# Kernel optimization log

Measured on AMD Instinct MI355X. Metric: run time of the kernel, lower is better.

The kernel has to match this reference:

```python
import jax, jax.numpy as jnp
import numpy as np

K = 3  # kernel_size


def conv2d_same(x, w, b):
    # x: NHWC, w: HWIO
    y = jax.lax.conv_general_dilated(
        x, w, window_strides=(1, 1), padding='SAME',
        dimension_numbers=('NHWC', 'HWIO', 'NHWC'))
    return y + b


def setup_inputs() -> dict:
    key = jax.random.key(0)
    k0, k1, k2 = jax.random.split(key, 3)
    B, H, Wd, C, F = 8, 128, 128, 64, 128
    x = jax.random.normal(k0, (B, H, Wd, C), jnp.float32)
    # offset conv: small random weights (zeros in original init -> degenerate),
    # scaled down so offsets stay in a realistic few-pixel range
    W_off = jax.random.normal(k1, (K, K, C, 2 * K * K), jnp.float32) * 0.01
    b_off = jnp.zeros((2 * K * K,), jnp.float32)
    fan_in = K * K * K * K * C
    W = jax.random.normal(k2, (K, K, K * K * C, F), jnp.float32) / np.float32(np.sqrt(fan_in))
    b = jnp.zeros((F,), jnp.float32)
    return {"x": x, "W_off": W_off, "b_off": b_off, "W": W, "b": b}


def reference(x, W_off, b_off, W, b):
    B, H, Wd, C = x.shape
    KK = K * K
    # predicted per-pixel, per-tap (dx, dy) offsets
    offsets = conv2d_same(x, W_off, b_off).reshape(B, H, Wd, KK, 2)

    # base pixel grid, stacked as (x, y) like the original
    gy, gx = jnp.meshgrid(jnp.arange(H, dtype=jnp.float32),
                          jnp.arange(Wd, dtype=jnp.float32), indexing='ij')
    grid = jnp.stack([gx, gy], axis=-1)[None, :, :, None, :]  # (1,H,W,1,2)

    # kernel tap grid, 'xy' meshgrid like tf.meshgrid default
    off = (K - 1) / 2.0
    lin = jnp.linspace(-off, off, K).astype(jnp.float32)
    kx, ky = jnp.meshgrid(lin, lin)
    kgrid = jnp.stack([kx, ky], axis=-1).reshape(1, 1, 1, KK, 2)

    loc = grid + kgrid + offsets  # (B,H,W,KK,2)
    lx = jnp.clip(loc[..., 0], 0.0, Wd - 1.0)
    ly = jnp.clip(loc[..., 1], 0.0, H - 1.0)

    x0 = jnp.clip(jnp.floor(lx), 0.0, Wd - 1.0)
    x1 = jnp.clip(jnp.floor(lx) + 1.0, 0.0, Wd - 1.0)
    y0 = jnp.clip(jnp.floor(ly), 0.0, H - 1.0)
    y1 = jnp.clip(jnp.floor(ly) + 1.0, 0.0, H - 1.0)

    # weights computed from the CLIPPED corner coords, as in the original
    wa = (x1 - lx) * (y1 - ly)
    wb = (x1 - lx) * (ly - y0)
    wc = (lx - x0) * (y1 - ly)
    wd = (lx - x0) * (ly - y0)

    x0i, x1i = x0.astype(jnp.int32), x1.astype(jnp.int32)
    y0i, y1i = y0.astype(jnp.int32), y1.astype(jnp.int32)

    xf = x.reshape(B, H * Wd, C)

    def gather(yi, xi):
        idx = (yi * Wd + xi).reshape(B, -1)           # (B, H*W*KK)
        g = jax.vmap(lambda f, i: f[i])(xf, idx)      # (B, P, C)
        return g.reshape(B, H, Wd, KK, C)

    Ia = gather(y0i, x0i)
    Ib = gather(y1i, x0i)
    Ic = gather(y0i, x1i)
    Id = gather(y1i, x1i)

    sampled = (wa[..., None] * Ia + wb[..., None] * Ib
               + wc[..., None] * Ic + wd[..., None] * Id)
    sampled = sampled.reshape(B, H, Wd, KK * C)
    return conv2d_same(sampled, W, b)
```

## Files before the change

kernel.cpp:

```cpp
#include <hip/hip_runtime.h>
#include <hip/hip_bf16.h>

#define B_   8
#define H_   128
#define W_   128
#define C_   64
#define F_   128
#define KDIM 5184
#define BHW_ 131072

#define TH   8
#define TW   16
#define HY   10
#define HX   18
#define NPX  180

#define STILE 0
#define BTILE 11520
#define PARMW 36096
#define PARMO 37536
#define LDSSZ 38976

typedef __bf16 bf16x8 __attribute__((ext_vector_type(8)));
typedef float  f32x4  __attribute__((ext_vector_type(4)));

__device__ __forceinline__ unsigned short f2bf(float f) {
  unsigned int u = __float_as_uint(f);
  unsigned int r = (u + 0x7fffu + ((u >> 16) & 1u)) >> 16;
  return (unsigned short)r;
}

__global__ __launch_bounds__(256) void woff_prep_kernel(
    const float* __restrict__ Woff, unsigned short* __restrict__ WbHi,
    unsigned short* __restrict__ WbLo) {
  int u = blockIdx.x * 256 + threadIdx.x;
  if (u >= 18432) return;
  int j  = u & 7;
  int kq = (u >> 3) & 3;
  int n  = (u >> 5) & 15;
  int nt = (u >> 9) & 1;
  int tc = u >> 10;
  int tap = tc >> 1, kch = tc & 1;
  int o = nt * 16 + n;
  int c = kch * 32 + kq * 8 + j;
  float val = 0.f;
  if (o < 18) val = Woff[(tap * 64 + c) * 18 + o];
  unsigned short h = f2bf(val);
  float hf = __uint_as_float((unsigned)h << 16);
  WbHi[u] = h;
  WbLo[u] = f2bf(val - hf);
}

__global__ __launch_bounds__(256, 3) void offs_mfma_kernel(
    const float* __restrict__ x, const unsigned short* __restrict__ WbHi,
    const unsigned short* __restrict__ WbLo, const float* __restrict__ boff,
    float* __restrict__ offsP) {
  __shared__ __align__(16) short lds[26112];
  const int tid = threadIdx.x, lane = tid & 63, w = tid >> 6;
  const int bid = blockIdx.x;
  const int b  = bid >> 7;
  const int t  = bid & 127;
  const int r4 = t >> 2, cq = t & 3;
  const int gy0 = r4 * 4, gx0 = cq * 32;
  const float* xb = x + (size_t)b * (H_ * W_ * C_);

#pragma unroll
  for (int it = 0; it < 7; ++it) {
    int u = it * 256 + tid;
    if (u < 1632) {
      int p = u >> 3, j = u & 7;
      int rowi = p / 34, coli = p - rowi * 34;
      int gy = gy0 - 1 + rowi, gx = gx0 - 1 + coli;
      union { unsigned short s[8]; uint4 v; } hi, lo;
      if ((unsigned)gy < (unsigned)H_ && (unsigned)gx < (unsigned)W_) {
        const float* src = xb + (((gy << 7) + gx) << 6) + j * 8;
        float4 v0 = ((const float4*)src)[0], v1 = ((const float4*)src)[1];
        float f[8] = {v0.x, v0.y, v0.z, v0.w, v1.x, v1.y, v1.z, v1.w};
#pragma unroll
        for (int e = 0; e < 8; ++e) {
          unsigned short h16 = f2bf(f[e]);
          hi.s[e] = h16;
          lo.s[e] = f2bf(f[e] - __uint_as_float((unsigned)h16 << 16));
        }
      } else {
        hi.v = make_uint4(0, 0, 0, 0);
        lo.v = hi.v;
      }
      int a = p * 64 + ((j ^ (coli & 7)) * 8);
      *(uint4*)&lds[a] = hi.v;
      *(uint4*)&lds[13056 + a] = lo.v;
    }
  }
  __syncthreads();

  const int l15 = lane & 15, kq = lane >> 4;
  const int bbase = (l15 * 4 + kq) * 8;
  f32x4 acc[2][2] = {};

#pragma unroll
  for (int ky = 0; ky < 3; ++ky) {
#pragma unroll
    for (int kx = 0; kx < 3; ++kx) {
      const int tap = ky * 3 + kx;
#pragma unroll
      for (int kch = 0; kch < 2; ++kch) {
        const int tc = tap * 2 + kch;
        bf16x8 bh0 = *(const bf16x8*)&WbHi[tc * 1024 + bbase];
        bf16x8 bh1 = *(const bf16x8*)&WbHi[tc * 1024 + 512 + bbase];
        bf16x8 bl0 = *(const bf16x8*)&WbLo[tc * 1024 + bbase];
        bf16x8 bl1 = *(const bf16x8*)&WbLo[tc * 1024 + 512 + bbase];
#pragma unroll
        for (int mt = 0; mt < 2; ++mt) {
          int coli = mt * 16 + l15 + kx;
          int px = (w + ky) * 34 + coli;
          int a = px * 64 + (((kch * 4 + kq) ^ (coli & 7)) * 8);
          bf16x8 ah = *(const bf16x8*)&lds[a];
          bf16x8 al = *(const bf16x8*)&lds[13056 + a];
          acc[mt][0] = __builtin_amdgcn_mfma_f32_16x16x32_bf16(ah, bh0, acc[mt][0], 0, 0, 0);
          acc[mt][0] = __builtin_amdgcn_mfma_f32_16x16x32_bf16(al, bh0, acc[mt][0], 0, 0, 0);
          acc[mt][0] = __builtin_amdgcn_mfma_f32_16x16x32_bf16(ah, bl0, acc[mt][0], 0, 0, 0);
          acc[mt][1] = __builtin_amdgcn_mfma_f32_16x16x32_bf16(ah, bh1, acc[mt][1], 0, 0, 0);
          acc[mt][1] = __builtin_amdgcn_mfma_f32_16x16x32_bf16(al, bh1, acc[mt][1], 0, 0, 0);
          acc[mt][1] = __builtin_amdgcn_mfma_f32_16x16x32_bf16(ah, bl1, acc[mt][1], 0, 0, 0);
        }
      }
    }
  }

  __syncthreads();
  float* accbuf = (float*)lds;
  float bv0 = boff[l15];
  float bv1 = boff[min(16 + l15, 17)];
#pragma unroll
  for (int mt = 0; mt < 2; ++mt)
#pragma unroll
    for (int r = 0; r < 4; ++r) {
      int px = mt * 16 + kq * 4 + r;
      accbuf[(w * 32 + px) * 19 + l15] = acc[mt][0][r] + bv0;
      if (l15 < 2)
        accbuf[(w * 32 + px) * 19 + 16 + l15] = acc[mt][1][r] + bv1;
    }
  __syncthreads();
  const int lane32 = tid & 31, tpi = tid >> 5;
#pragma unroll
  for (int v = 0; v < 9; ++v) {
    int u = v * 8 + tpi;
    int o = u >> 2, w2 = u & 3;
    float val = accbuf[(w2 * 32 + lane32) * 19 + o];
    offsP[(size_t)o * BHW_ + (size_t)b * 16384 + (gy0 + w2) * 128 + gx0 + lane32] = val;
  }
}

__global__ __launch_bounds__(256) void wt_prep_kernel(
    const float* __restrict__ Wf, unsigned short* __restrict__ Wt) {
  __shared__ float Wl[64][65];
  const int tid = threadIdx.x;
  const int kk0 = (blockIdx.x % 81) * 64;
  const int f0  = (blockIdx.x / 81) * 64;
  for (int i = tid; i < 4096; i += 256) {
    int kk = i >> 6, f = i & 63;
    Wl[kk][f] = Wf[(size_t)(kk0 + kk) * F_ + f0 + f];
  }
  __syncthreads();
  for (int i = tid; i < 4096; i += 256) {
    int f = i >> 6, kk = i & 63;
    Wt[(size_t)(f0 + f) * KDIM + kk0 + kk] = f2bf(Wl[kk][f]);
  }
}

__global__ __launch_bounds__(256, 2) void fused_kernel(
    const float* __restrict__ x, const float* __restrict__ offsP,
    const unsigned short* __restrict__ Wt, const float* __restrict__ bias,
    float* __restrict__ out) {
  __shared__ __align__(16) short lds[LDSSZ];
  const int tid  = threadIdx.x;
  const int lane = tid & 63;
  const int wv   = tid >> 6;
  const int gr   = (blockIdx.x & 7) * 128 + (blockIdx.x >> 3);
  const int b    = gr >> 7;
  const int tile = gr & 127;
  const int ty   = tile >> 3, tx = tile & 7;
  const int gy0  = ty * TH, gx0 = tx * TW;
  const float* xb = x + (size_t)b * (H_ * W_ * C_);

  const int l15  = lane & 15, quad = lane >> 4;
  const int sub  = lane & 7,  rig  = lane >> 3;
  const int wn   = (wv & 1) * 64;

  f32x4 acc[4][4] = {};

  int p0[4];
#pragma unroll
  for (int i = 0; i < 4; ++i) p0[i] = ((wv >> 1) * 4 + i) * HX + l15;
  int bo[2][4];
#pragma unroll
  for (int ks = 0; ks < 2; ++ks)
#pragma unroll
    for (int j = 0; j < 4; ++j)
      bo[ks][j] = BTILE + (wn + 16 * j + l15) * 64 + (((ks * 4 + quad) ^ (l15 & 7)) * 8);

  const int s_py = tid / HX, s_px = tid - s_py * HX;

  for (int t = 0; t < 9; ++t) {
    __syncthreads();
#pragma unroll
    for (int i = 0; i < 12; ++i) {
      int slot = wv * 12 + i;
      int chunk = slot >> 4;
      int f = ((slot & 15) * 8) + rig;
      const short* src = (const short*)Wt + (size_t)f * KDIM +
                         chunk * 576 + t * 64 + ((sub ^ rig) * 8);
      __builtin_amdgcn_global_load_lds(
          (const __attribute__((address_space(1))) void*)src,
          (__attribute__((address_space(3))) void*)&lds[BTILE + slot * 512],
          16, 0, 0);
    }
    if (tid < NPX) {
      int gy = gy0 + s_py - 1, gx = gx0 + s_px - 1;
      float wa = 0.f, wb = 0.f, wc = 0.f, wd = 0.f;
      int oA = 0, oB = 0, oC = 0, oD = 0;
      if ((unsigned)gy < (unsigned)H_ && (unsigned)gx < (unsigned)W_) {
        int pix = (b * H_ + gy) * W_ + gx;
        float offx = offsP[(size_t)(2 * t) * BHW_ + pix];
        float offy = offsP[(size_t)(2 * t + 1) * BHW_ + pix];
        float lx = (float)gx + (float)(t % 3 - 1) + offx;
        float ly = (float)gy + (float)(t / 3 - 1) + offy;
        lx = fminf(fmaxf(lx, 0.f), 127.f);
        ly = fminf(fmaxf(ly, 0.f), 127.f);
        float fx = floorf(lx), fy = floorf(ly);
        float x0c = fminf(fmaxf(fx, 0.f), 127.f);
        float x1c = fminf(fmaxf(fx + 1.f, 0.f), 127.f);
        float y0c = fminf(fmaxf(fy, 0.f), 127.f);
        float y1c = fminf(fmaxf(fy + 1.f, 0.f), 127.f);
        wa = (x1c - lx) * (y1c - ly);
        wb = (x1c - lx) * (ly - y0c);
        wc = (lx - x0c) * (y1c - ly);
        wd = (lx - x0c) * (ly - y0c);
        int ix0 = (int)x0c, ix1 = (int)x1c, iy0 = (int)y0c, iy1 = (int)y1c;
        oA = (iy0 * W_ + ix0) * C_;
        oB = (iy1 * W_ + ix0) * C_;
        oC = (iy0 * W_ + ix1) * C_;
        oD = (iy1 * W_ + ix1) * C_;
      }
      ((float4*)&lds[PARMW])[tid] = make_float4(wa, wb, wc, wd);
      ((int4*)&lds[PARMO])[tid]  = make_int4(oA | (s_px << 20), oB, oC, oD);
    }
    __syncthreads();
#pragma unroll
    for (int it = 0; it < 6; ++it) {
      int u = it * 256 + tid;
      if (u < NPX * 8) {
        int p = u >> 3, j = u & 7;
        float4 wv4 = ((const float4*)&lds[PARMW])[p];
        int4   ov4 = ((const int4*)&lds[PARMO])[p];
        int pxl = ov4.x >> 20;
        const float* pa = xb + (ov4.x & 0xFFFFF) + j * 8;
        const float* pb = xb + ov4.y + j * 8;
        const float* pc = xb + ov4.z + j * 8;
        const float* pd = xb + ov4.w + j * 8;
        float4 A0 = ((const float4*)pa)[0], A1 = ((const float4*)pa)[1];
        float4 B0 = ((const float4*)pb)[0], B1 = ((const float4*)pb)[1];
        float4 C0 = ((const float4*)pc)[0], C1 = ((const float4*)pc)[1];
        float4 D0 = ((const float4*)pd)[0], D1 = ((const float4*)pd)[1];
        union { __bf16 h[8]; uint4 v; } uu;
        uu.h[0] = (__bf16)(wv4.x * A0.x + wv4.y * B0.x + wv4.z * C0.x + wv4.w * D0.x);
        uu.h[1] = (__bf16)(wv4.x * A0.y + wv4.y * B0.y + wv4.z * C0.y + wv4.w * D0.y);
        uu.h[2] = (__bf16)(wv4.x * A0.z + wv4.y * B0.z + wv4.z * C0.z + wv4.w * D0.z);
        uu.h[3] = (__bf16)(wv4.x * A0.w + wv4.y * B0.w + wv4.z * C0.w + wv4.w * D0.w);
        uu.h[4] = (__bf16)(wv4.x * A1.x + wv4.y * B1.x + wv4.z * C1.x + wv4.w * D1.x);
        uu.h[5] = (__bf16)(wv4.x * A1.y + wv4.y * B1.y + wv4.z * C1.y + wv4.w * D1.y);
        uu.h[6] = (__bf16)(wv4.x * A1.z + wv4.y * B1.z + wv4.z * C1.z + wv4.w * D1.z);
        uu.h[7] = (__bf16)(wv4.x * A1.w + wv4.y * B1.w + wv4.z * C1.w + wv4.w * D1.w);
        *(uint4*)&lds[STILE + p * 64 + ((j ^ (pxl & 7)) * 8)] = uu.v;
      }
    }
    __syncthreads();

    for (int g = 0; g < 3; ++g) {
      const int off2 = g * HX;
#pragma unroll
      for (int c3 = 0; c3 < 3; ++c3) {
        int t1 = (l15 + c3) & 7;
        int xr0 = ((quad ^ t1) * 8);
        int xr1 = (((4 + quad) ^ t1) * 8);
#pragma unroll
        for (int ks = 0; ks < 2; ++ks) {
          int xr = ks ? xr1 : xr0;
          bf16x8 af[4], bfr[4];
#pragma unroll
          for (int i = 0; i < 4; ++i)
            af[i] = *(const bf16x8*)&lds[(p0[i] + off2 + c3) * 64 + xr];
#pragma unroll
          for (int j = 0; j < 4; ++j)
            bfr[j] = *(const bf16x8*)&lds[bo[ks][j] + c3 * 8192];
#pragma unroll
          for (int i = 0; i < 4; ++i)
#pragma unroll
            for (int j = 0; j < 4; ++j)
              acc[i][j] = __builtin_amdgcn_mfma_f32_16x16x32_bf16(
                  af[i], bfr[j], acc[i][j], 0, 0, 0);
        }
      }
      if (g < 2) {
        __syncthreads();
#pragma unroll
        for (int i = 0; i < 12; ++i) {
          int slot = wv * 12 + i;
          int chunk = slot >> 4;
          int f = ((slot & 15) * 8) + rig;
          int tap2 = (g + 1) * 3 + chunk;
          const short* src = (const short*)Wt + (size_t)f * KDIM +
                             tap2 * 576 + t * 64 + ((sub ^ rig) * 8);
          __builtin_amdgcn_global_load_lds(
              (const __attribute__((address_space(1))) void*)src,
              (__attribute__((address_space(3))) void*)&lds[BTILE + slot * 512],
              16, 0, 0);
        }
        __syncthreads();
      }
    }
  }

  float bj[4];
#pragma unroll
  for (int j = 0; j < 4; ++j) bj[j] = bias[wn + 16 * j + l15];
#pragma unroll
  for (int i = 0; i < 4; ++i) {
    int gy = gy0 + (wv >> 1) * 4 + i;
#pragma unroll
    for (int r = 0; r < 4; ++r) {
      int gx = gx0 + quad * 4 + r;
      float* rp = out + ((size_t)((b * H_ + gy) * W_ + gx)) * F_;
#pragma unroll
      for (int j = 0; j < 4; ++j)
        rp[wn + 16 * j + l15] = acc[i][j][r] + bj[j];
    }
  }
}

extern "C" void kernel_launch(void* const* d_in, const int* in_sizes, int n_in,
                              void* d_out, int out_size, void* d_ws, size_t ws_size,
                              hipStream_t stream) {
  (void)in_sizes; (void)n_in; (void)out_size; (void)ws_size;
  const float* x    = (const float*)d_in[0];
  const float* Woff = (const float*)d_in[1];
  const float* boff = (const float*)d_in[2];
  const float* Wf   = (const float*)d_in[3];
  const float* bias = (const float*)d_in[4];
  float* out = (float*)d_out;

  char* ws = (char*)d_ws;
  size_t off_bytes = (size_t)18 * BHW_ * 4;
  size_t p1 = (off_bytes + 255) & ~(size_t)255;
  size_t wt_bytes = (size_t)F_ * KDIM * 2;
  float*          offsP = (float*)ws;
  unsigned short* Wt    = (unsigned short*)(ws + p1);
  unsigned short* WbHi  = (unsigned short*)(ws + p1 + wt_bytes);
  unsigned short* WbLo  = WbHi + 18432;

  woff_prep_kernel<<<72, 256, 0, stream>>>(Woff, WbHi, WbLo);
  offs_mfma_kernel<<<1024, 256, 0, stream>>>(x, WbHi, WbLo, boff, offsP);
  wt_prep_kernel<<<162, 256, 0, stream>>>(Wf, Wt);
  fused_kernel<<<1024, 256, 0, stream>>>(x, offsP, Wt, bias, out);
}
```

Measured before the change: 297.1 us.

## Stream weight tiles per wave with triple-buffered async loads, drop block barriers

Weight staging in the fused kernel changes from block-wide 3-tap chunks, each fenced by two __syncthreads, to per-wave private triple-buffered LDS slots. Each wave loads only the 64 output channels it needs, one 32-channel sub-tile at a time, and keeps the loads two steps ahead using explicit vmcnt waits and s_setprio around the MFMAs. This is meant to remove the block barriers inside the MFMA loop and overlap global-to-LDS weight traffic with compute. The trade-offs are duplicated weight loads across waves that share output channels, and fragile hand-counted vmcnt values. The offset prep kernel also switches to native bf16 casts instead of manual rounding.

Result: slower. 312.6 us (+5.2%).

```diff
diff --git a/kernel.cpp b/kernel.cpp
--- a/kernel.cpp
+++ b/kernel.cpp
@@ -16,7 +16,7 @@
 #define NPX  180
 
 #define STILE 0
-#define BTILE 11520
+#define BT    11520
 #define PARMW 36096
 #define PARMO 37536
 #define LDSSZ 38976
@@ -71,16 +71,16 @@
       int p = u >> 3, j = u & 7;
       int rowi = p / 34, coli = p - rowi * 34;
       int gy = gy0 - 1 + rowi, gx = gx0 - 1 + coli;
-      union { unsigned short s[8]; uint4 v; } hi, lo;
+      union { __bf16 h[8]; uint4 v; } hi, lo;
       if ((unsigned)gy < (unsigned)H_ && (unsigned)gx < (unsigned)W_) {
         const float* src = xb + (((gy << 7) + gx) << 6) + j * 8;
         float4 v0 = ((const float4*)src)[0], v1 = ((const float4*)src)[1];
         float f[8] = {v0.x, v0.y, v0.z, v0.w, v1.x, v1.y, v1.z, v1.w};
 #pragma unroll
         for (int e = 0; e < 8; ++e) {
-          unsigned short h16 = f2bf(f[e]);
-          hi.s[e] = h16;
-          lo.s[e] = f2bf(f[e] - __uint_as_float((unsigned)h16 << 16));
+          __bf16 h16 = (__bf16)f[e];
+          hi.h[e] = h16;
+          lo.h[e] = (__bf16)(f[e] - (float)h16);
         }
       } else {
         hi.v = make_uint4(0, 0, 0, 0);
@@ -167,6 +167,21 @@
     Wt[(size_t)(f0 + f) * KDIM + kk0 + kk] = f2bf(Wl[kk][f]);
   }
 }
+
+#define STAGE_SUB(tt, tp2, fsv, bufv)                                          \
+  do {                                                                         \
+    _Pragma("unroll")                                                          \
+    for (int li_ = 0; li_ < 4; ++li_) {                                        \
+      int f_ = wn + (fsv) * 32 + li_ * 8 + rig;                                \
+      const short* src_ = (const short*)Wt + (size_t)f_ * KDIM +               \
+                          (tp2) * 576 + (tt) * 64 + ((sub ^ rig) * 8);         \
+      __builtin_amdgcn_global_load_lds(                                        \
+          (const __attribute__((address_space(1))) void*)src_,                 \
+          (__attribute__((address_space(3))) void*)                            \
+              &lds[wbase + (bufv) * 2048 + li_ * 512],                         \
+          16, 0, 0);                                                           \
+    }                                                                          \
+  } while (0)
 
 __global__ __launch_bounds__(256, 2) void fused_kernel(
     const float* __restrict__ x, const float* __restrict__ offsP,
@@ -186,35 +201,24 @@
   const int l15  = lane & 15, quad = lane >> 4;
   const int sub  = lane & 7,  rig  = lane >> 3;
   const int wn   = (wv & 1) * 64;
+  const int wbase = BT + wv * 6144;
 
   f32x4 acc[4][4] = {};
 
   int p0[4];
 #pragma unroll
   for (int i = 0; i < 4; ++i) p0[i] = ((wv >> 1) * 4 + i) * HX + l15;
-  int bo[2][4];
+  int bo2[2][2];
 #pragma unroll
   for (int ks = 0; ks < 2; ++ks)
 #pragma unroll
-    for (int j = 0; j < 4; ++j)
-      bo[ks][j] = BTILE + (wn + 16 * j + l15) * 64 + (((ks * 4 + quad) ^ (l15 & 7)) * 8);
+    for (int j2 = 0; j2 < 2; ++j2)
+      bo2[ks][j2] = (16 * j2 + l15) * 64 + (((ks * 4 + quad) ^ (l15 & 7)) * 8);
 
   const int s_py = tid / HX, s_px = tid - s_py * HX;
 
   for (int t = 0; t < 9; ++t) {
     __syncthreads();
-#pragma unroll
-    for (int i = 0; i < 12; ++i) {
-      int slot = wv * 12 + i;
-      int chunk = slot >> 4;
-      int f = ((slot & 15) * 8) + rig;
-      const short* src = (const short*)Wt + (size_t)f * KDIM +
-                         chunk * 576 + t * 64 + ((sub ^ rig) * 8);
-      __builtin_amdgcn_global_load_lds(
-          (const __attribute__((address_space(1))) void*)src,
-          (__attribute__((address_space(3))) void*)&lds[BTILE + slot * 512],
-          16, 0, 0);
-    }
     if (tid < NPX) {
       int gy = gy0 + s_py - 1, gx = gx0 + s_px - 1;
       float wa = 0.f, wb = 0.f, wc = 0.f, wd = 0.f;
@@ -246,6 +250,8 @@
       ((int4*)&lds[PARMO])[tid]  = make_int4(oA | (s_px << 20), oB, oC, oD);
     }
     __syncthreads();
+    STAGE_SUB(t, 0, 0, 0);
+    STAGE_SUB(t, 0, 1, 1);
 #pragma unroll
     for (int it = 0; it < 6; ++it) {
       int u = it * 256 + tid;
@@ -276,47 +282,42 @@
     }
     __syncthreads();
 
-    for (int g = 0; g < 3; ++g) {
-      const int off2 = g * HX;
-#pragma unroll
-      for (int c3 = 0; c3 < 3; ++c3) {
-        int t1 = (l15 + c3) & 7;
-        int xr0 = ((quad ^ t1) * 8);
-        int xr1 = (((4 + quad) ^ t1) * 8);
+#pragma unroll
+    for (int tap2 = 0; tap2 < 9; ++tap2) {
+      const int g = tap2 / 3, c3 = tap2 % 3;
+      const int t1 = (l15 + c3) & 7;
+      bf16x8 af[2][4];
+#pragma unroll
+      for (int ks = 0; ks < 2; ++ks)
+#pragma unroll
+        for (int i = 0; i < 4; ++i)
+          af[ks][i] = *(const bf16x8*)&lds[(p0[i] + g * HX + c3) * 64 +
+                                           (((ks * 4 + quad) ^ t1) * 8)];
+#pragma unroll
+      for (int fs = 0; fs < 2; ++fs) {
+        const int s = tap2 * 2 + fs;
+        if (s <= 15) {
+          STAGE_SUB(t, (s + 2) >> 1, (s + 2) & 1, (s + 2) % 3);
+        }
+        if (s < 16)        asm volatile("s_waitcnt vmcnt(8)" ::: "memory");
+        else if (s == 16)  asm volatile("s_waitcnt vmcnt(4)" ::: "memory");
+        else               asm volatile("s_waitcnt vmcnt(0)" ::: "memory");
+        __builtin_amdgcn_sched_barrier(0);
+        const int cb = wbase + (s % 3) * 2048;
+        __builtin_amdgcn_s_setprio(1);
 #pragma unroll
         for (int ks = 0; ks < 2; ++ks) {
-          int xr = ks ? xr1 : xr0;
-          bf16x8 af[4], bfr[4];
-#pragma unroll
-          for (int i = 0; i < 4; ++i)
-            af[i] = *(const bf16x8*)&lds[(p0[i] + off2 + c3) * 64 + xr];
-#pragma unroll
-          for (int j = 0; j < 4; ++j)
-            bfr[j] = *(const bf16x8*)&lds[bo[ks][j] + c3 * 8192];
-#pragma unroll
-          for (int i = 0; i < 4; ++i)
-#pragma unroll
-            for (int j = 0; j < 4; ++j)
-              acc[i][j] = __builtin_amdgcn_mfma_f32_16x16x32_bf16(
-                  af[i], bfr[j], acc[i][j], 0, 0, 0);
+          bf16x8 b0 = *(const bf16x8*)&lds[cb + bo2[ks][0]];
+          bf16x8 b1 = *(const bf16x8*)&lds[cb + bo2[ks][1]];
+#pragma unroll
+          for (int i = 0; i < 4; ++i) {
+            acc[i][fs * 2 + 0] = __builtin_amdgcn_mfma_f32_16x16x32_bf16(
+                af[ks][i], b0, acc[i][fs * 2 + 0], 0, 0, 0);
+            acc[i][fs * 2 + 1] = __builtin_amdgcn_mfma_f32_16x16x32_bf16(
+                af[ks][i], b1, acc[i][fs * 2 + 1], 0, 0, 0);
+          }
         }
-      }
-      if (g < 2) {
-        __syncthreads();
-#pragma unroll
-        for (int i = 0; i < 12; ++i) {
-          int slot = wv * 12 + i;
-          int chunk = slot >> 4;
-          int f = ((slot & 15) * 8) + rig;
-          int tap2 = (g + 1) * 3 + chunk;
-          const short* src = (const short*)Wt + (size_t)f * KDIM +
-                             tap2 * 576 + t * 64 + ((sub ^ rig) * 8);
-          __builtin_amdgcn_global_load_lds(
-              (const __attribute__((address_space(1))) void*)src,
-              (__attribute__((address_space(3))) void*)&lds[BTILE + slot * 512],
-              16, 0, 0);
-        }
-        __syncthreads();
+        __builtin_amdgcn_s_setprio(0);
       }
     }
   }
```
